# Performance work log

Hardware: AMD Instinct MI355X
Metric: run time of the kernel (lower is better)

Reference implementation:

```python
import jax, jax.numpy as jnp
import numpy as np

NUM_TYPES = 4
EPS = 1e-5
NEG_SLOPE = 0.01  # nn.LeakyReLU default


def hetero_linear(x, node_type, W, b):
    # x: [N, Cin], W: [T, Cin, Cout], b: [T, Cout]
    # Grouped GEMM via type-masked batched matmul (T is small and fixed).
    onehot = jax.nn.one_hot(node_type, NUM_TYPES, dtype=x.dtype)  # [N, T]
    xt = onehot.T[:, :, None] * x[None, :, :]                      # [T, N, Cin]
    y = jnp.einsum('tni,tio->no', xt, W)                           # [N, Cout]
    return y + b[node_type]


def hetero_batchnorm(x, node_type, gamma, beta):
    # Per-type batch statistics over the nodes of each type (training-mode BN).
    ones = jnp.ones((x.shape[0],), dtype=x.dtype)
    cnt = jax.ops.segment_sum(ones, node_type, num_segments=NUM_TYPES)      # [T]
    cnt = jnp.maximum(cnt, 1.0)
    s = jax.ops.segment_sum(x, node_type, num_segments=NUM_TYPES)           # [T, C]
    ss = jax.ops.segment_sum(x * x, node_type, num_segments=NUM_TYPES)      # [T, C]
    mean = s / cnt[:, None]
    var = ss / cnt[:, None] - mean * mean  # biased variance, as BN uses
    xn = (x - mean[node_type]) * jax.lax.rsqrt(var[node_type] + EPS)
    return xn * gamma[node_type] + beta[node_type]


def setup_inputs() -> dict:
    key = jax.random.key(0)
    ks = jax.random.split(key, 12)
    N, CIN, H, COUT, T = 32768, 256, 512, 256, NUM_TYPES
    x = jax.random.normal(ks[0], (N, CIN), dtype=jnp.float32)
    node_type = jax.random.randint(ks[1], (N,), 0, T, dtype=jnp.int32)
    def lin(k, ci, co):
        k1, k2 = jax.random.split(k)
        scale = 1.0 / np.sqrt(ci)
        W = jax.random.uniform(k1, (T, ci, co), jnp.float32, -scale, scale)
        b = jax.random.uniform(k2, (T, co), jnp.float32, -scale, scale)
        return W, b
    W1, b1 = lin(ks[2], CIN, H)
    W2, b2 = lin(ks[3], H, H)
    W3, b3 = lin(ks[4], H, COUT)
    gamma1 = jnp.ones((T, H), jnp.float32)
    beta1 = jnp.zeros((T, H), jnp.float32)
    gamma2 = jnp.ones((T, H), jnp.float32)
    beta2 = jnp.zeros((T, H), jnp.float32)
    return {"x": x, "node_type": node_type,
            "W1": W1, "b1": b1, "W2": W2, "b2": b2, "W3": W3, "b3": b3,
            "gamma1": gamma1, "beta1": beta1, "gamma2": gamma2, "beta2": beta2}


def reference(x, node_type, W1, b1, W2, b2, W3, b3, gamma1, beta1, gamma2, beta2):
    # Layer 1: HeteroLinear -> HeteroBatchNorm -> LeakyReLU (dropout p=0 -> identity)
    h = hetero_linear(x, node_type, W1, b1)
    h = hetero_batchnorm(h, node_type, gamma1, beta1)
    h = jax.nn.leaky_relu(h, NEG_SLOPE)
    # Layer 2
    h = hetero_linear(h, node_type, W2, b2)
    h = hetero_batchnorm(h, node_type, gamma2, beta2)
    h = jax.nn.leaky_relu(h, NEG_SLOPE)
    # Layer 3: plain_last -> no norm/act
    out = hetero_linear(h, node_type, W3, b3)
    return out
```

## Files before the change

kernel.cpp:

```cpp
#include <hip/hip_runtime.h>
#include <cstdint>
#include <cstddef>

#define N_NODES 32768
#define CIN 256
#define HDIM 512
#define COUT_F 256
#define NTYPE 4
#define ALIGN_SEG 128
#define NPAD (N_NODES + NTYPE * ALIGN_SEG)
#define NROWBLK (NPAD / 128)
#define BN_EPS 1e-5f
#define SLOPE 0.01f

typedef unsigned short u16;
typedef __attribute__((ext_vector_type(8))) short bf16x8;
typedef __attribute__((ext_vector_type(4))) float f32x4;
typedef __attribute__((ext_vector_type(4))) u16 u16x4;

#define GLOBAL_AS __attribute__((address_space(1)))
#define LDS_AS __attribute__((address_space(3)))

__device__ __forceinline__ u16 f2bf(float f) {
  union { float f; unsigned u; } v{f};
  unsigned r = (v.u + 0x7FFF + ((v.u >> 16) & 1)) >> 16;
  return (u16)r;
}
__device__ __forceinline__ float bf2f(u16 b) {
  union { unsigned u; float f; } v;
  v.u = ((unsigned)b) << 16;
  return v.f;
}


__global__ void hist_kernel(const int* __restrict__ nt, int* __restrict__ blockHist) {
  __shared__ int h[NTYPE];
  int tid = threadIdx.x;
  if (tid < NTYPE) h[tid] = 0;
  __syncthreads();
  int i = blockIdx.x * 256 + tid;
  atomicAdd(&h[nt[i]], 1);
  __syncthreads();
  if (tid < NTYPE) blockHist[blockIdx.x * NTYPE + tid] = h[tid];
}

__global__ void scan_kernel(const int* __restrict__ blockHist, int* __restrict__ blockBase,
                            int* __restrict__ meta) {
  int tid = threadIdx.x;
  if (tid < NTYPE) {
    int run = 0;
    for (int b = 0; b < 128; ++b) {
      blockBase[b * NTYPE + tid] = run;
      run += blockHist[b * NTYPE + tid];
    }
    meta[tid] = run;
  }
  __syncthreads();
  if (tid == 0) {
    int s = 0;
    for (int t = 0; t < NTYPE; ++t) {
      meta[4 + t] = s;
      s += (meta[t] + ALIGN_SEG - 1) & ~(ALIGN_SEG - 1);
    }
    meta[8] = s;
  }
}

__global__ void rank_scatter_kernel(const int* __restrict__ nt, const int* __restrict__ blockBase,
                                    const int* __restrict__ meta, int* __restrict__ perm) {
  __shared__ int st[256];
  int tid = threadIdx.x;
  int i = blockIdx.x * 256 + tid;
  int t = nt[i];
  st[tid] = t;
  __syncthreads();
  int rank = 0;
  for (int j = 0; j < tid; ++j) rank += (st[j] == t) ? 1 : 0;
  perm[meta[4 + t] + blockBase[blockIdx.x * NTYPE + t] + rank] = i;
}

__global__ void gather_kernel(const float* __restrict__ x, const int* __restrict__ perm,
                              u16* __restrict__ xs) {
  int p = blockIdx.x;
  int src = perm[p];
  u16x4* dst = (u16x4*)(xs + (size_t)p * CIN);
  if (src < 0) {
    dst[threadIdx.x] = (u16x4)0;
  } else {
    float4 v = ((const float4*)(x + (size_t)src * CIN))[threadIdx.x];
    u16x4 o;
    o.x = f2bf(v.x); o.y = f2bf(v.y); o.z = f2bf(v.z); o.w = f2bf(v.w);
    dst[threadIdx.x] = o;
  }
}

template <int K, int COUT>
__global__ __launch_bounds__(256) void wtrans_kernel(const float* __restrict__ W,
                                                     u16* __restrict__ Wt) {
  const int t = blockIdx.z;
  const int k0 = blockIdx.x * 32, c0 = blockIdx.y * 32;
  const float* __restrict__ Ws = W + (size_t)t * K * COUT;
  u16* __restrict__ Wd = Wt + (size_t)t * COUT * K;
  __shared__ float tile[32][33];
  int tid = threadIdx.x;
#pragma unroll
  for (int p = 0; p < 4; ++p) {
    int idx = p * 256 + tid;
    int r = idx >> 5, c = idx & 31;
    tile[r][c] = Ws[(size_t)(k0 + r) * COUT + c0 + c];
  }
  __syncthreads();
#pragma unroll
  for (int p = 0; p < 4; ++p) {
    int idx = p * 256 + tid;
    int r = idx >> 5, c = idx & 31;
    Wd[(size_t)(c0 + r) * K + k0 + c] = f2bf(tile[c][r]);
  }
}


template <int K, int COUT, bool SCATTER, bool STATS>
__global__ __launch_bounds__(256) void mfma_gemm_kernel(
    const u16* __restrict__ A, const u16* __restrict__ Wt, const float* __restrict__ bias,
    u16* __restrict__ Yb, float* __restrict__ Yf, float* __restrict__ partS,
    float* __restrict__ partQ, const int* __restrict__ meta, const int* __restrict__ perm) {
  const int col0 = blockIdx.x * 128, row0 = blockIdx.y * 128;
  const int s1 = meta[5], s2 = meta[6], s3 = meta[7];
  const int t = row0 >= s3 ? 3 : (row0 >= s2 ? 2 : (row0 >= s1 ? 1 : 0));
  const int seg_end = meta[4 + t] + meta[t];
  const u16* __restrict__ Bt = Wt + (size_t)t * COUT * K;

  __shared__ __align__(16) u16 As[128 * 64];
  __shared__ __align__(16) u16 Bs[128 * 64];

  const int tid = threadIdx.x;
  const int lane = tid & 63;
  const int lr = lane & 15, ls = lane >> 4;
  const int wid = tid >> 6;
  const int wm = wid >> 1, wn = wid & 1;

  int a_off[4][2], b_off[4][2];
#pragma unroll
  for (int i = 0; i < 4; ++i) {
    int r = wm * 64 + i * 16 + lr;
#pragma unroll
    for (int kk = 0; kk < 2; ++kk) a_off[i][kk] = r * 64 + (((kk * 4 + ls)) ^ (r & 7)) * 8;
  }
#pragma unroll
  for (int j = 0; j < 4; ++j) {
    int r = wn * 64 + j * 16 + lr;
#pragma unroll
    for (int kk = 0; kk < 2; ++kk) b_off[j][kk] = r * 64 + (((kk * 4 + ls)) ^ (r & 7)) * 8;
  }

  int st_row[4], st_col[4];
#pragma unroll
  for (int p = 0; p < 4; ++p) {
    int l = p * 256 + tid;
    int r = l >> 3, u = l & 7;
    st_row[p] = r;
    st_col[p] = (u ^ (r & 7)) * 8;
  }
  const int lds_base = (tid & 192) * 8;

  f32x4 acc[4][4] = {};

  for (int k0 = 0; k0 < K; k0 += 64) {
#pragma unroll
    for (int p = 0; p < 4; ++p) {
      const u16* ga = A + (size_t)(row0 + st_row[p]) * K + k0 + st_col[p];
      const u16* gb = Bt + (size_t)(col0 + st_row[p]) * K + k0 + st_col[p];
      __builtin_amdgcn_global_load_lds((const GLOBAL_AS void*)ga,
                                       (LDS_AS void*)(As + p * 2048 + lds_base), 16, 0, 0);
      __builtin_amdgcn_global_load_lds((const GLOBAL_AS void*)gb,
                                       (LDS_AS void*)(Bs + p * 2048 + lds_base), 16, 0, 0);
    }
    __syncthreads();
#pragma unroll
    for (int kk = 0; kk < 2; ++kk) {
      bf16x8 af[4], bfr[4];
#pragma unroll
      for (int i = 0; i < 4; ++i) af[i] = *(const bf16x8*)(As + a_off[i][kk]);
#pragma unroll
      for (int j = 0; j < 4; ++j) bfr[j] = *(const bf16x8*)(Bs + b_off[j][kk]);
#pragma unroll
      for (int i = 0; i < 4; ++i)
#pragma unroll
        for (int j = 0; j < 4; ++j)
          acc[i][j] = __builtin_amdgcn_mfma_f32_16x16x32_bf16(af[i], bfr[j], acc[i][j], 0, 0, 0);
    }
    __syncthreads();
  }

  float bj[4];
#pragma unroll
  for (int j = 0; j < 4; ++j) bj[j] = bias[(size_t)t * COUT + col0 + wn * 64 + j * 16 + lr];

  if (SCATTER) {
#pragma unroll
    for (int i = 0; i < 4; ++i) {
      int rbase = row0 + wm * 64 + i * 16 + ls * 4;
      int dsts[4];
#pragma unroll
      for (int r = 0; r < 4; ++r) dsts[r] = perm[rbase + r];
#pragma unroll
      for (int j = 0; j < 4; ++j) {
        int gcol = col0 + wn * 64 + j * 16 + lr;
#pragma unroll
        for (int r = 0; r < 4; ++r) {
          if (dsts[r] >= 0) Yf[(size_t)dsts[r] * COUT + gcol] = acc[i][j][r] + bj[j];
        }
      }
    }
  } else {
    float s[4] = {}, q[4] = {};
#pragma unroll
    for (int i = 0; i < 4; ++i) {
      int rbase = row0 + wm * 64 + i * 16 + ls * 4;
#pragma unroll
      for (int j = 0; j < 4; ++j) {
        int gcol = col0 + wn * 64 + j * 16 + lr;
#pragma unroll
        for (int r = 0; r < 4; ++r) {
          int row = rbase + r;
          float y = acc[i][j][r] + bj[j];
          Yb[(size_t)row * COUT + gcol] = f2bf(y);
          if (STATS && row < seg_end) {
            s[j] += y;
            q[j] += y * y;
          }
        }
      }
    }
    if (STATS) {
      float* sred = (float*)As;
      float* qred = (float*)Bs;
      int slot = (wm * 4 + ls) * 128 + wn * 64 + lr;
#pragma unroll
      for (int j = 0; j < 4; ++j) {
        sred[slot + j * 16] = s[j];
        qred[slot + j * 16] = q[j];
      }
      __syncthreads();
      if (tid < 128) {
        float S = 0.f, Q = 0.f;
#pragma unroll
        for (int k = 0; k < 8; ++k) {
          S += sred[k * 128 + tid];
          Q += qred[k * 128 + tid];
        }
        partS[(size_t)blockIdx.y * COUT + col0 + tid] = S;
        partQ[(size_t)blockIdx.y * COUT + col0 + tid] = Q;
      }
    }
  }
}


__global__ __launch_bounds__(256) void bn_finalize_kernel(const float* __restrict__ partS,
                                                          const float* __restrict__ partQ,
                                                          const int* __restrict__ meta,
                                                          float* __restrict__ mean,
                                                          float* __restrict__ rstd) {
  int idx = blockIdx.x * 256 + threadIdx.x;
  int t = idx >> 9;
  int c = idx & (HDIM - 1);
  int start = meta[4 + t];
  int cnt = meta[t];
  int b0 = start >> 7;
  int nb = (cnt + 127) >> 7;
  float S = 0.f, Q = 0.f;
  for (int b = 0; b < nb; ++b) {
    S += partS[(size_t)(b0 + b) * HDIM + c];
    Q += partQ[(size_t)(b0 + b) * HDIM + c];
  }
  float n = (float)(cnt > 1 ? cnt : 1);
  float m = S / n;
  float var = Q / n - m * m;
  mean[idx] = m;
  rstd[idx] = rsqrtf(fmaxf(var, 0.f) + BN_EPS);
}


__global__ __launch_bounds__(256) void bn_apply_kernel(
    const u16* __restrict__ h, const int* __restrict__ meta, const float* __restrict__ mean,
    const float* __restrict__ rstd, const float* __restrict__ gamma,
    const float* __restrict__ beta, u16* __restrict__ aout) {
  int idx = blockIdx.x * 256 + threadIdx.x;
  int row = idx >> 6;
  int g8 = (idx & 63) * 8;
  const int s1 = meta[5], s2 = meta[6], s3 = meta[7];
  const int t = row >= s3 ? 3 : (row >= s2 ? 2 : (row >= s1 ? 1 : 0));
  size_t base = (size_t)row * HDIM + g8;
  uint4 v = *(const uint4*)(h + base);
  unsigned w[4] = {v.x, v.y, v.z, v.w};
  int tb = t * HDIM + g8;
  float mv[8], rv[8], gv[8], bv[8];
  *(float4*)&mv[0] = *(const float4*)(mean + tb);
  *(float4*)&mv[4] = *(const float4*)(mean + tb + 4);
  *(float4*)&rv[0] = *(const float4*)(rstd + tb);
  *(float4*)&rv[4] = *(const float4*)(rstd + tb + 4);
  *(float4*)&gv[0] = *(const float4*)(gamma + tb);
  *(float4*)&gv[4] = *(const float4*)(gamma + tb + 4);
  *(float4*)&bv[0] = *(const float4*)(beta + tb);
  *(float4*)&bv[4] = *(const float4*)(beta + tb + 4);
  unsigned o[4];
#pragma unroll
  for (int p = 0; p < 4; ++p) {
    u16 lo = (u16)(w[p] & 0xFFFF), hi = (u16)(w[p] >> 16);
    int e0 = p * 2, e1 = p * 2 + 1;
    float sc0 = rv[e0] * gv[e0], sc1 = rv[e1] * gv[e1];
    float y0 = bf2f(lo) * sc0 + (bv[e0] - mv[e0] * sc0);
    float y1 = bf2f(hi) * sc1 + (bv[e1] - mv[e1] * sc1);
    y0 = y0 >= 0.f ? y0 : SLOPE * y0;
    y1 = y1 >= 0.f ? y1 : SLOPE * y1;
    o[p] = (unsigned)f2bf(y0) | ((unsigned)f2bf(y1) << 16);
  }
  *(uint4*)(aout + base) = make_uint4(o[0], o[1], o[2], o[3]);
}


extern "C" void kernel_launch(void* const* d_in, const int* in_sizes, int n_in, void* d_out,
                              int out_size, void* d_ws, size_t ws_size, hipStream_t stream) {
  const float* x = (const float*)d_in[0];
  const int* nt = (const int*)d_in[1];
  const float* W1 = (const float*)d_in[2];
  const float* b1 = (const float*)d_in[3];
  const float* W2 = (const float*)d_in[4];
  const float* b2 = (const float*)d_in[5];
  const float* W3 = (const float*)d_in[6];
  const float* b3 = (const float*)d_in[7];
  const float* g1 = (const float*)d_in[8];
  const float* be1 = (const float*)d_in[9];
  const float* g2 = (const float*)d_in[10];
  const float* be2 = (const float*)d_in[11];
  float* out = (float*)d_out;

  char* ws = (char*)d_ws;
  size_t off = 0;
  auto alloc = [&](size_t bytes) {
    void* p = ws + off;
    off = (off + bytes + 255) & ~(size_t)255;
    return p;
  };
  int* meta = (int*)alloc(16 * 4);
  int* blockHist = (int*)alloc(128 * NTYPE * 4);
  int* blockBase = (int*)alloc(128 * NTYPE * 4);
  int* perm = (int*)alloc((size_t)NPAD * 4);
  float* mean = (float*)alloc((size_t)NTYPE * HDIM * 4);
  float* rstd = (float*)alloc((size_t)NTYPE * HDIM * 4);
  float* partS = (float*)alloc((size_t)NROWBLK * HDIM * 4);
  float* partQ = (float*)alloc((size_t)NROWBLK * HDIM * 4);
  u16* Wt1 = (u16*)alloc((size_t)NTYPE * CIN * HDIM * 2);
  u16* Wt2 = (u16*)alloc((size_t)NTYPE * HDIM * HDIM * 2);
  u16* Wt3 = (u16*)alloc((size_t)NTYPE * HDIM * COUT_F * 2);
  u16* xs = (u16*)alloc((size_t)NPAD * CIN * 2);
  u16* abuf = (u16*)alloc((size_t)NPAD * HDIM * 2);
  u16* hb = (u16*)alloc((size_t)NPAD * HDIM * 2);

  hipMemsetAsync(meta, 0, 64, stream);
  hipMemsetAsync(perm, 0xFF, (size_t)NPAD * 4, stream);
  hist_kernel<<<128, 256, 0, stream>>>(nt, blockHist);
  scan_kernel<<<1, 64, 0, stream>>>(blockHist, blockBase, meta);
  rank_scatter_kernel<<<128, 256, 0, stream>>>(nt, blockBase, meta, perm);
  gather_kernel<<<NPAD, 64, 0, stream>>>(x, perm, xs);

  wtrans_kernel<CIN, HDIM><<<dim3(CIN / 32, HDIM / 32, NTYPE), 256, 0, stream>>>(W1, Wt1);
  wtrans_kernel<HDIM, HDIM><<<dim3(HDIM / 32, HDIM / 32, NTYPE), 256, 0, stream>>>(W2, Wt2);
  wtrans_kernel<HDIM, COUT_F><<<dim3(HDIM / 32, COUT_F / 32, NTYPE), 256, 0, stream>>>(W3, Wt3);

  mfma_gemm_kernel<CIN, HDIM, false, true><<<dim3(HDIM / 128, NPAD / 128), 256, 0, stream>>>(
      xs, Wt1, b1, hb, nullptr, partS, partQ, meta, nullptr);
  bn_finalize_kernel<<<(NTYPE * HDIM) / 256, 256, 0, stream>>>(partS, partQ, meta, mean, rstd);
  bn_apply_kernel<<<(NPAD * (HDIM / 8)) / 256, 256, 0, stream>>>(hb, meta, mean, rstd, g1, be1,
                                                                 abuf);
  mfma_gemm_kernel<HDIM, HDIM, false, true><<<dim3(HDIM / 128, NPAD / 128), 256, 0, stream>>>(
      abuf, Wt2, b2, hb, nullptr, partS, partQ, meta, nullptr);
  bn_finalize_kernel<<<(NTYPE * HDIM) / 256, 256, 0, stream>>>(partS, partQ, meta, mean, rstd);
  bn_apply_kernel<<<(NPAD * (HDIM / 8)) / 256, 256, 0, stream>>>(hb, meta, mean, rstd, g2, be2,
                                                                 abuf);
  mfma_gemm_kernel<HDIM, COUT_F, true, false><<<dim3(COUT_F / 128, NPAD / 128), 256, 0, stream>>>(
      abuf, Wt3, b3, nullptr, out, nullptr, nullptr, meta, perm);
}
```

Baseline: 194.8 us.

## Double-buffer GEMM LDS tiles, remap workgroups for locality, batch gather rows

The MFMA GEMM now uses two LDS buffers so the global-to-LDS loads for the next K tile are issued before the MFMAs on the current tile. It waits with explicit vmcnt counts and raw barriers in place of full syncthreads. Workgroup IDs are remapped with an XCD-style interleave so neighbouring tiles share L2, and launch bounds ask for two blocks per CU. The gather kernel handles four rows per 256-thread block instead of one row per 64-thread block. LDS use doubles to 64KB per block, which may limit occupancy, and the hand-written waitcnt logic is fragile.

```diff
diff --git a/kernel.cpp b/kernel.cpp
--- a/kernel.cpp
+++ b/kernel.cpp
@@ -79,18 +79,20 @@
   perm[meta[4 + t] + blockBase[blockIdx.x * NTYPE + t] + rank] = i;
 }
 
-__global__ void gather_kernel(const float* __restrict__ x, const int* __restrict__ perm,
-                              u16* __restrict__ xs) {
-  int p = blockIdx.x;
+__global__ __launch_bounds__(256) void gather_kernel(const float* __restrict__ x,
+                                                     const int* __restrict__ perm,
+                                                     u16* __restrict__ xs) {
+  int p = blockIdx.x * 4 + (threadIdx.x >> 6);
+  int lane = threadIdx.x & 63;
   int src = perm[p];
   u16x4* dst = (u16x4*)(xs + (size_t)p * CIN);
   if (src < 0) {
-    dst[threadIdx.x] = (u16x4)0;
+    dst[lane] = (u16x4)0;
   } else {
-    float4 v = ((const float4*)(x + (size_t)src * CIN))[threadIdx.x];
+    float4 v = ((const float4*)(x + (size_t)src * CIN))[lane];
     u16x4 o;
     o.x = f2bf(v.x); o.y = f2bf(v.y); o.z = f2bf(v.z); o.w = f2bf(v.w);
-    dst[threadIdx.x] = o;
+    dst[lane] = o;
   }
 }
 
@@ -120,18 +122,24 @@
 
 
 template <int K, int COUT, bool SCATTER, bool STATS>
-__global__ __launch_bounds__(256) void mfma_gemm_kernel(
+__global__ __launch_bounds__(256, 2) void mfma_gemm_kernel(
     const u16* __restrict__ A, const u16* __restrict__ Wt, const float* __restrict__ bias,
     u16* __restrict__ Yb, float* __restrict__ Yf, float* __restrict__ partS,
     float* __restrict__ partQ, const int* __restrict__ meta, const int* __restrict__ perm) {
-  const int col0 = blockIdx.x * 128, row0 = blockIdx.y * 128;
+  constexpr int GX = COUT / 128;
+  const int nwg = (int)(gridDim.x * gridDim.y);
+  int l = (int)(blockIdx.y * gridDim.x + blockIdx.x);
+  int lid = (l & 7) * (nwg >> 3) + (l >> 3);
+  const int bx = lid % GX, by = lid / GX;
+  const int col0 = bx * 128, row0 = by * 128;
+
   const int s1 = meta[5], s2 = meta[6], s3 = meta[7];
   const int t = row0 >= s3 ? 3 : (row0 >= s2 ? 2 : (row0 >= s1 ? 1 : 0));
   const int seg_end = meta[4 + t] + meta[t];
   const u16* __restrict__ Bt = Wt + (size_t)t * COUT * K;
 
-  __shared__ __align__(16) u16 As[128 * 64];
-  __shared__ __align__(16) u16 Bs[128 * 64];
+  __shared__ __align__(16) u16 As[2][128 * 64];
+  __shared__ __align__(16) u16 Bs[2][128 * 64];
 
   const int tid = threadIdx.x;
   const int lane = tid & 63;
@@ -156,40 +164,54 @@
   int st_row[4], st_col[4];
 #pragma unroll
   for (int p = 0; p < 4; ++p) {
-    int l = p * 256 + tid;
-    int r = l >> 3, u = l & 7;
+    int lch = p * 256 + tid;
+    int r = lch >> 3, u = lch & 7;
     st_row[p] = r;
     st_col[p] = (u ^ (r & 7)) * 8;
   }
   const int lds_base = (tid & 192) * 8;
 
-  f32x4 acc[4][4] = {};
-
-  for (int k0 = 0; k0 < K; k0 += 64) {
+  const int nt = K / 64;
+
+  auto stage = [&](int buf, int k0) {
 #pragma unroll
     for (int p = 0; p < 4; ++p) {
       const u16* ga = A + (size_t)(row0 + st_row[p]) * K + k0 + st_col[p];
       const u16* gb = Bt + (size_t)(col0 + st_row[p]) * K + k0 + st_col[p];
       __builtin_amdgcn_global_load_lds((const GLOBAL_AS void*)ga,
-                                       (LDS_AS void*)(As + p * 2048 + lds_base), 16, 0, 0);
+                                       (LDS_AS void*)(&As[buf][0] + p * 2048 + lds_base), 16, 0, 0);
       __builtin_amdgcn_global_load_lds((const GLOBAL_AS void*)gb,
-                                       (LDS_AS void*)(Bs + p * 2048 + lds_base), 16, 0, 0);
-    }
-    __syncthreads();
+                                       (LDS_AS void*)(&Bs[buf][0] + p * 2048 + lds_base), 16, 0, 0);
+    }
+  };
+
+  f32x4 acc[4][4] = {};
+
+  stage(0, 0);
+  for (int t8 = 0; t8 < nt; ++t8) {
+    const int cur = t8 & 1;
+    if (t8 + 1 < nt) {
+      stage(cur ^ 1, (t8 + 1) * 64);
+      asm volatile("s_waitcnt vmcnt(8)" ::: "memory");
+    } else {
+      asm volatile("s_waitcnt vmcnt(0)" ::: "memory");
+    }
+    __builtin_amdgcn_s_barrier();
+    __builtin_amdgcn_sched_barrier(0);
 #pragma unroll
     for (int kk = 0; kk < 2; ++kk) {
       bf16x8 af[4], bfr[4];
 #pragma unroll
-      for (int i = 0; i < 4; ++i) af[i] = *(const bf16x8*)(As + a_off[i][kk]);
-#pragma unroll
-      for (int j = 0; j < 4; ++j) bfr[j] = *(const bf16x8*)(Bs + b_off[j][kk]);
+      for (int i = 0; i < 4; ++i) af[i] = *(const bf16x8*)(&As[cur][0] + a_off[i][kk]);
+#pragma unroll
+      for (int j = 0; j < 4; ++j) bfr[j] = *(const bf16x8*)(&Bs[cur][0] + b_off[j][kk]);
 #pragma unroll
       for (int i = 0; i < 4; ++i)
 #pragma unroll
         for (int j = 0; j < 4; ++j)
           acc[i][j] = __builtin_amdgcn_mfma_f32_16x16x32_bf16(af[i], bfr[j], acc[i][j], 0, 0, 0);
     }
-    __syncthreads();
+    __builtin_amdgcn_s_barrier();
   }
 
   float bj[4];
@@ -233,9 +255,10 @@
       }
     }
     if (STATS) {
-      float* sred = (float*)As;
-      float* qred = (float*)Bs;
+      float* sred = (float*)&As[0][0];
+      float* qred = (float*)&Bs[0][0];
       int slot = (wm * 4 + ls) * 128 + wn * 64 + lr;
+      __syncthreads();
 #pragma unroll
       for (int j = 0; j < 4; ++j) {
         sred[slot + j * 16] = s[j];
@@ -249,8 +272,8 @@
           S += sred[k * 128 + tid];
           Q += qred[k * 128 + tid];
         }
-        partS[(size_t)blockIdx.y * COUT + col0 + tid] = S;
-        partQ[(size_t)blockIdx.y * COUT + col0 + tid] = Q;
+        partS[(size_t)by * COUT + col0 + tid] = S;
+        partQ[(size_t)by * COUT + col0 + tid] = Q;
       }
     }
   }
@@ -363,7 +386,7 @@
   hist_kernel<<<128, 256, 0, stream>>>(nt, blockHist);
   scan_kernel<<<1, 64, 0, stream>>>(blockHist, blockBase, meta);
   rank_scatter_kernel<<<128, 256, 0, stream>>>(nt, blockBase, meta, perm);
-  gather_kernel<<<NPAD, 64, 0, stream>>>(x, perm, xs);
+  gather_kernel<<<NPAD / 4, 256, 0, stream>>>(x, perm, xs);
 
   wtrans_kernel<CIN, HDIM><<<dim3(CIN / 32, HDIM / 32, NTYPE), 256, 0, stream>>>(W1, Wt1);
   wtrans_kernel<HDIM, HDIM><<<dim3(HDIM / 32, HDIM / 32, NTYPE), 256, 0, stream>>>(W2, Wt2);
```

Measured after the change: 179.9 us. -7.7%, faster.
